# Optimization experiments

Measured on AMD Instinct MI355X. Metric: run time of the kernel, lower is better.

The kernel has to match this reference:

```python
import jax, jax.numpy as jnp
import numpy as np

BLOCK_SIZE = 64
NUM_STEPS = 3
# pad_type='post', init_type='ones', attention_mask=None


def setup_inputs() -> dict:
    key = jax.random.key(0)
    k1, k2, k3 = jax.random.split(key, 3)
    B, H, S, D = 4, 16, 4096, 64
    return {
        "query": jax.random.normal(k1, (B, H, S, D), dtype=jnp.float32),
        "key": jax.random.normal(k2, (B, H, S, D), dtype=jnp.float32),
        "value": jax.random.normal(k3, (B, H, S, D), dtype=jnp.float32),
    }


def _soba_monarch(query, key, value):
    B, H, S, D = query.shape
    bs = BLOCK_SIZE
    nb = -(-S // bs)                 # ceil(S / bs)
    pad = nb * bs - S                # post padding amount
    q = query / (D ** 0.5)

    pad_cfg = ((0, 0), (0, 0), (0, pad), (0, 0))
    Qb = jnp.pad(q, pad_cfg).reshape(B, H, nb, bs, D)      # (l j) v -> l j v
    Kb = jnp.pad(key, pad_cfg).reshape(B, H, nb, bs, D)    # (k i) v -> k i v

    # validity of positions in the padded sequence (post-pad)
    pos_valid = (jnp.arange(nb * bs) < S).reshape(nb, bs)  # [block, within]
    # left factor shape (..., j, l, k): rows of the flattened (l j) axis
    left_mask = jnp.broadcast_to(pos_valid.T[:, :, None], (bs, nb, nb))      # j l k
    # right factor shape (..., k, j, i): columns of the flattened (k i) axis
    right_mask = jnp.broadcast_to(pos_valid[:, None, :], (nb, bs, bs))       # k j i

    NEG = jnp.finfo(q.dtype).min
    # init_type = 'ones'
    left = jnp.broadcast_to(
        jnp.where(left_mask, 1.0 / nb, 0.0), (B, H, bs, nb, nb)
    ).astype(q.dtype)

    for _ in range(NUM_STEPS):
        # beta[k,j,i] = sum_{l,v} left[j,l,k] Q[l,j,v] K[k,i,v]
        beta = jnp.einsum('bhjlk,bhljv,bhkiv->bhkji', left, Qb, Kb, optimize=True)
        tau = jnp.swapaxes(jnp.sum(left, axis=-2), -1, -2)[..., None]        # bhkj1
        tau_zero = jnp.isclose(tau, 0.0)
        tau_safe = jnp.where(tau_zero, 1.0, tau)
        logits_r = jnp.where(right_mask & ~tau_zero, beta / tau_safe, NEG)
        right = jax.nn.softmax(logits_r, axis=-1)
        right = jnp.where(right_mask, right, 0.0)

        # alpha[j,1,k] = sum_i right[k,j,i] log right[k,j,i]  (xlogy)
        r_safe = jnp.where(right > 0, right, 1.0)
        alpha = jnp.sum(right * jnp.log(r_safe), axis=-1)                    # bhkj
        alpha = jnp.swapaxes(alpha, -1, -2)[..., None, :]                    # bhj1k

        beta2 = jnp.einsum('bhkji,bhljv,bhkiv->bhjlk', right, Qb, Kb, optimize=True)
        left = jax.nn.softmax(jnp.where(left_mask, beta2 - alpha, NEG), axis=-1)
        left = jnp.where(left_mask, left, 0.0)

    # multiply: z = L (R V)
    Vb = jnp.pad(value, pad_cfg).reshape(B, H, nb, bs, D)                    # k i v
    Y = jnp.einsum('bhkji,bhkiv->bhkjv', right, Vb)
    Z = jnp.einsum('bhjlk,bhkjv->bhljv', left, Y)
    z = Z.reshape(B, H, nb * bs, D)
    return z[..., :S, :]


def reference(query, key, value):
    return _soba_monarch(query, key, value)
```

## Files before the change

kernel.cpp:

```cpp
#include <hip/hip_runtime.h>


namespace {

typedef __attribute__((ext_vector_type(8))) short short8v;
typedef __attribute__((ext_vector_type(4))) float f32x4;
typedef __attribute__((ext_vector_type(4))) uint uint4v;

constexpr int HEADS = 64;
constexpr size_t HEADQ = 262144;
constexpr size_t MATF  = (size_t)HEADS * 262144;

#define MFMA(ACC, A, B) ACC = __builtin_amdgcn_mfma_f32_16x16x32_bf16(A, B, ACC, 0, 0, 0)

__device__ __forceinline__ float rmax16(float m) {
    m = fmaxf(m, __shfl_xor(m, 1));
    m = fmaxf(m, __shfl_xor(m, 2));
    m = fmaxf(m, __shfl_xor(m, 4));
    m = fmaxf(m, __shfl_xor(m, 8));
    return m;
}
__device__ __forceinline__ float rsum16(float s) {
    s += __shfl_xor(s, 1);
    s += __shfl_xor(s, 2);
    s += __shfl_xor(s, 4);
    s += __shfl_xor(s, 8);
    return s;
}

__device__ __forceinline__ uint packbf(float x) {
    uint u = __float_as_uint(x);
    uint hi = (u + 0x7FFFu + ((u >> 16) & 1u)) & 0xFFFF0000u;
    float d = x - __uint_as_float(hi);
    return hi | (__float_as_uint(d) >> 16);
}

__device__ __forceinline__ void fragpair(const uint* T, int row, int g8,
                                         short8v& h, short8v& l) {
    const uint* p = T + row * 68 + g8 * 8;
    uint4 a = *(const uint4*)(p);
    uint4 b = *(const uint4*)(p + 4);
    uint h01 = (a.x >> 16) | (a.y & 0xFFFF0000u);
    uint h23 = (a.z >> 16) | (a.w & 0xFFFF0000u);
    uint h45 = (b.x >> 16) | (b.y & 0xFFFF0000u);
    uint h67 = (b.z >> 16) | (b.w & 0xFFFF0000u);
    uint l01 = (a.x & 0xFFFFu) | (a.y << 16);
    uint l23 = (a.z & 0xFFFFu) | (a.w << 16);
    uint l45 = (b.x & 0xFFFFu) | (b.y << 16);
    uint l67 = (b.z & 0xFFFFu) | (b.w << 16);
    h = __builtin_bit_cast(short8v, (uint4v){h01, h23, h45, h67});
    l = __builtin_bit_cast(short8v, (uint4v){l01, l23, l45, l67});
}

__global__ void kmean_kernel(const float* __restrict__ Q, uint* __restrict__ M) {
    const int wg = blockIdx.x;
    const int h  = wg >> 6, j = wg & 63;
    const int v  = threadIdx.x;
    const float* base = Q + (size_t)h * HEADQ + (size_t)j * 64 + v;
    float acc = 0.f;
    #pragma unroll
    for (int l = 0; l < 64; ++l) acc += base[(size_t)l * 4096];
    M[(size_t)wg * 64 + v] = packbf(acc * (1.0f / 512.0f));
}

template<int FIRST, int LAST>
__global__ __launch_bounds__(256) void bc_kernel(
    const uint*  __restrict__ Gsrc,
    const float* __restrict__ Kmat,
    const float* __restrict__ Vmat,
    const float* __restrict__ tauIn,
    float* __restrict__ Hm,
    float* __restrict__ alphaOut,
    float* __restrict__ Yout)
{
    __shared__ uint sG[64 * 68];
    __shared__ uint sK[64 * 68];
    __shared__ uint sT[64 * 68];

    const int wg = blockIdx.x, h = wg >> 6, k = wg & 63;
    const int tid = threadIdx.x;
    const int r = tid & 63, c0 = (tid >> 6) << 4;

    {
        const uint* gp = Gsrc + (FIRST ? (size_t)h * 4096 : (size_t)wg * 4096) + r * 64 + c0;
        uint* d = sG + r * 68 + c0;
        #pragma unroll
        for (int q = 0; q < 4; ++q) *(uint4*)(d + 4 * q) = *(const uint4*)(gp + 4 * q);
    }
    {
        const float* kp = Kmat + (size_t)h * HEADQ + (size_t)k * 4096 + r * 64 + c0;
        uint pk[16];
        #pragma unroll
        for (int q = 0; q < 4; ++q) {
            float4 f = *(const float4*)(kp + 4 * q);
            pk[4*q+0] = packbf(f.x); pk[4*q+1] = packbf(f.y);
            pk[4*q+2] = packbf(f.z); pk[4*q+3] = packbf(f.w);
        }
        uint* d = sK + r * 68 + c0;
        #pragma unroll
        for (int q = 0; q < 4; ++q)
            *(uint4*)(d + 4 * q) = *(const uint4*)(&pk[4 * q]);
        #pragma unroll
        for (int e = 0; e < 16; ++e) sT[(c0 + e) * 68 + r] = pk[e];
    }
    float vf[16];
    if (LAST) {
        const float* vp = Vmat + (size_t)h * HEADQ + (size_t)k * 4096 + r * 64 + c0;
        #pragma unroll
        for (int q = 0; q < 4; ++q) {
            float4 f = *(const float4*)(vp + 4 * q);
            vf[4*q+0] = f.x; vf[4*q+1] = f.y; vf[4*q+2] = f.z; vf[4*q+3] = f.w;
        }
    }
    __syncthreads();

    const int w = tid >> 6, lo4 = tid & 15, hi4 = (tid >> 4) & 3;

    f32x4 acc[4] = {};
    #pragma unroll
    for (int ks = 0; ks < 2; ++ks) {
        short8v ah, al; fragpair(sG, 16 * w + lo4, hi4 + 4 * ks, ah, al);
        #pragma unroll
        for (int t = 0; t < 4; ++t) {
            short8v bh, bl; fragpair(sK, 16 * t + lo4, hi4 + 4 * ks, bh, bl);
            MFMA(acc[t], ah, bh); MFMA(acc[t], ah, bl); MFMA(acc[t], al, bh);
        }
    }
    __syncthreads();

    float tvv[4];
    #pragma unroll
    for (int rr = 0; rr < 4; ++rr)
        tvv[rr] = FIRST ? 1.0f : tauIn[(size_t)wg * 64 + 16 * w + 4 * hi4 + rr];

    #pragma unroll
    for (int rr = 0; rr < 4; ++rr) {
        const int j = 16 * w + 4 * hi4 + rr;
        const bool tz = !(tvv[rr] > 1e-8f);
        const float tvi = tz ? 1.0f : (1.0f / tvv[rr]);
        float lg[4];
        #pragma unroll
        for (int t = 0; t < 4; ++t) lg[t] = acc[t][rr] * tvi;
        float m = fmaxf(fmaxf(lg[0], lg[1]), fmaxf(lg[2], lg[3]));
        m = rmax16(m);
        float e[4], s = 0.f;
        #pragma unroll
        for (int t = 0; t < 4; ++t) { e[t] = __expf(lg[t] - m); s += e[t]; }
        s = rsum16(s);
        const float inv = 1.0f / s;
        float ap = 0.f;
        #pragma unroll
        for (int t = 0; t < 4; ++t) {
            const float rrv = tz ? (1.0f / 64.0f) : e[t] * inv;
            ap += (rrv > 0.f) ? rrv * __logf(rrv) : 0.f;
            sG[j * 68 + 16 * t + lo4] = packbf(rrv);
        }
        ap = rsum16(ap);
        if (lo4 == 0) alphaOut[(size_t)wg * 64 + j] = ap;
    }
    if (LAST) {
        #pragma unroll
        for (int e = 0; e < 16; ++e) sK[(c0 + e) * 68 + r] = packbf(vf[e]);
    }
    __syncthreads();

    f32x4 acc2[4] = {};
    f32x4 acc3[4] = {};
    #pragma unroll
    for (int ks = 0; ks < 2; ++ks) {
        short8v ah, al; fragpair(sG, 16 * w + lo4, hi4 + 4 * ks, ah, al);
        #pragma unroll
        for (int t = 0; t < 4; ++t) {
            short8v bh, bl; fragpair(sT, 16 * t + lo4, hi4 + 4 * ks, bh, bl);
            MFMA(acc2[t], ah, bh); MFMA(acc2[t], ah, bl); MFMA(acc2[t], al, bh);
            if (LAST) {
                short8v ch, cl; fragpair(sK, 16 * t + lo4, hi4 + 4 * ks, ch, cl);
                MFMA(acc3[t], ah, ch); MFMA(acc3[t], ah, cl); MFMA(acc3[t], al, ch);
            }
        }
    }
    #pragma unroll
    for (int rr = 0; rr < 4; ++rr) {
        const int j = 16 * w + 4 * hi4 + rr;
        const size_t base = (size_t)h * 262144 + (size_t)j * 4096 + (size_t)k * 64;
        #pragma unroll
        for (int t = 0; t < 4; ++t) {
            Hm[base + 16 * t + lo4] = acc2[t][rr];
            if (LAST) Yout[base + 16 * t + lo4] = acc3[t][rr];
        }
    }
}

template<int LAST>
__global__ __launch_bounds__(256) void da_kernel(
    const float* __restrict__ Q,
    const float* __restrict__ HmIn,
    const float* __restrict__ alphaIn,
    const float* __restrict__ Yin,
    uint*  __restrict__ Gout,
    float* __restrict__ tauOut,
    float* __restrict__ Zout)
{
    __shared__ uint sQ[64 * 68];
    __shared__ uint sH[64 * 68];
    __shared__ uint sT[64 * 68];

    const int wg = blockIdx.x, h = wg >> 6, j = wg & 63;
    const int tid = threadIdx.x;
    const int r = tid & 63, c0 = (tid >> 6) << 4;

    {
        const float* qp = Q + (size_t)h * HEADQ + (size_t)r * 4096 + (size_t)j * 64 + c0;
        uint pq[16];
        #pragma unroll
        for (int q = 0; q < 4; ++q) {
            float4 f = *(const float4*)(qp + 4 * q);
            pq[4*q+0] = packbf(f.x * 0.125f); pq[4*q+1] = packbf(f.y * 0.125f);
            pq[4*q+2] = packbf(f.z * 0.125f); pq[4*q+3] = packbf(f.w * 0.125f);
        }
        uint* d = sQ + r * 68 + c0;
        #pragma unroll
        for (int q = 0; q < 4; ++q)
            *(uint4*)(d + 4 * q) = *(const uint4*)(&pq[4 * q]);
        if (!LAST) {
            #pragma unroll
            for (int e = 0; e < 16; ++e) sT[(c0 + e) * 68 + r] = pq[e];
        }
    }
    {
        const float* hp = HmIn + (size_t)wg * 4096 + r * 64 + c0;
        uint ph[16];
        #pragma unroll
        for (int q = 0; q < 4; ++q) {
            float4 f = *(const float4*)(hp + 4 * q);
            ph[4*q+0] = packbf(f.x); ph[4*q+1] = packbf(f.y);
            ph[4*q+2] = packbf(f.z); ph[4*q+3] = packbf(f.w);
        }
        uint* d = sH + r * 68 + c0;
        #pragma unroll
        for (int q = 0; q < 4; ++q)
            *(uint4*)(d + 4 * q) = *(const uint4*)(&ph[4 * q]);
    }
    if (LAST) {
        const float* yp = Yin + (size_t)wg * 4096 + r * 64 + c0;
        float yf[16];
        #pragma unroll
        for (int q = 0; q < 4; ++q) {
            float4 f = *(const float4*)(yp + 4 * q);
            yf[4*q+0] = f.x; yf[4*q+1] = f.y; yf[4*q+2] = f.z; yf[4*q+3] = f.w;
        }
        #pragma unroll
        for (int e = 0; e < 16; ++e) sT[(c0 + e) * 68 + r] = packbf(yf[e]);
    }
    __syncthreads();

    const int w = tid >> 6, lo4 = tid & 15, hi4 = (tid >> 4) & 3;

    f32x4 acc[4] = {};
    #pragma unroll
    for (int ks = 0; ks < 2; ++ks) {
        short8v ah, al; fragpair(sQ, 16 * w + lo4, hi4 + 4 * ks, ah, al);
        #pragma unroll
        for (int t = 0; t < 4; ++t) {
            short8v bh, bl; fragpair(sH, 16 * t + lo4, hi4 + 4 * ks, bh, bl);
            MFMA(acc[t], ah, bh); MFMA(acc[t], ah, bl); MFMA(acc[t], al, bh);
        }
    }
    __syncthreads();

    float av[4];
    #pragma unroll
    for (int t = 0; t < 4; ++t)
        av[t] = alphaIn[((size_t)h * 64 + 16 * t + lo4) * 64 + j];

    #pragma unroll
    for (int rr = 0; rr < 4; ++rr) {
        const int l = 16 * w + 4 * hi4 + rr;
        float lg[4];
        #pragma unroll
        for (int t = 0; t < 4; ++t) lg[t] = acc[t][rr] - av[t];
        float m = fmaxf(fmaxf(lg[0], lg[1]), fmaxf(lg[2], lg[3]));
        m = rmax16(m);
        float e[4], s = 0.f;
        #pragma unroll
        for (int t = 0; t < 4; ++t) { e[t] = __expf(lg[t] - m); s += e[t]; }
        s = rsum16(s);
        const float inv = 1.0f / s;
        #pragma unroll
        for (int t = 0; t < 4; ++t) {
            const uint pv = packbf(e[t] * inv);
            if (!LAST) sH[(16 * t + lo4) * 68 + l] = pv;
            else       sH[l * 68 + 16 * t + lo4] = pv;
        }
    }
    __syncthreads();

    if (!LAST) {
        f32x4 acc2[4] = {};
        f32x4 tacc = {};
        short8v onesb;
        #pragma unroll
        for (int e = 0; e < 8; ++e) onesb[e] = (lo4 == 0) ? (short)0x3F80 : (short)0;
        #pragma unroll
        for (int ks = 0; ks < 2; ++ks) {
            short8v ah, al; fragpair(sH, 16 * w + lo4, hi4 + 4 * ks, ah, al);
            MFMA(tacc, ah, onesb); MFMA(tacc, al, onesb);
            #pragma unroll
            for (int t = 0; t < 4; ++t) {
                short8v bh, bl; fragpair(sT, 16 * t + lo4, hi4 + 4 * ks, bh, bl);
                MFMA(acc2[t], ah, bh); MFMA(acc2[t], ah, bl); MFMA(acc2[t], al, bh);
            }
        }
        #pragma unroll
        for (int rr = 0; rr < 4; ++rr) {
            const int kq = 16 * w + 4 * hi4 + rr;
            const size_t gb = ((size_t)h * 64 + kq) * 4096 + (size_t)j * 64;
            #pragma unroll
            for (int t = 0; t < 4; ++t) Gout[gb + 16 * t + lo4] = packbf(acc2[t][rr]);
            if (lo4 == 0) tauOut[((size_t)h * 64 + kq) * 64 + j] = tacc[rr];
        }
    } else {
        f32x4 acc2[4] = {};
        #pragma unroll
        for (int ks = 0; ks < 2; ++ks) {
            short8v ah, al; fragpair(sH, 16 * w + lo4, hi4 + 4 * ks, ah, al);
            #pragma unroll
            for (int t = 0; t < 4; ++t) {
                short8v bh, bl; fragpair(sT, 16 * t + lo4, hi4 + 4 * ks, bh, bl);
                MFMA(acc2[t], ah, bh); MFMA(acc2[t], ah, bl); MFMA(acc2[t], al, bh);
            }
        }
        #pragma unroll
        for (int rr = 0; rr < 4; ++rr) {
            const int l = 16 * w + 4 * hi4 + rr;
            const size_t zb = (size_t)h * HEADQ + (size_t)l * 4096 + (size_t)j * 64;
            #pragma unroll
            for (int t = 0; t < 4; ++t) Zout[zb + 16 * t + lo4] = acc2[t][rr];
        }
    }
}

}

extern "C" void kernel_launch(void* const* d_in, const int* in_sizes, int n_in,
                              void* d_out, int out_size, void* d_ws, size_t ws_size,
                              hipStream_t stream) {
    const float* Q = (const float*)d_in[0];
    const float* K = (const float*)d_in[1];
    const float* V = (const float*)d_in[2];
    float* out = (float*)d_out;

    char* ws = (char*)d_ws;
    const size_t MB = 1024 * 1024;
    uint*  G   = (uint*)(ws);
    float* Hm  = (float*)(ws + 64 * MB);
    uint*  M   = (uint*)(ws + 128 * MB);
    float* al  = (float*)(ws + 129 * MB);
    float* tau = (float*)(ws + 130 * MB);

    const bool bigws = ws_size >= (size_t)196 * MB;
    float* Ybuf = bigws ? (float*)(ws + 131 * MB) : out;
    float* Zdst = bigws ? out : (float*)G;

    dim3 blk(256), grid(HEADS * 64);

    kmean_kernel<<<dim3(HEADS * 64), dim3(64), 0, stream>>>(Q, M);
    bc_kernel<1, 0><<<grid, blk, 0, stream>>>(M, K, nullptr, nullptr, Hm, al, nullptr);
    da_kernel<0>   <<<grid, blk, 0, stream>>>(Q, Hm, al, nullptr, G, tau, nullptr);
    bc_kernel<0, 0><<<grid, blk, 0, stream>>>(G, K, nullptr, tau, Hm, al, nullptr);
    da_kernel<0>   <<<grid, blk, 0, stream>>>(Q, Hm, al, nullptr, G, tau, nullptr);
    bc_kernel<0, 1><<<grid, blk, 0, stream>>>(G, K, V, tau, Hm, al, Ybuf);
    da_kernel<1>   <<<grid, blk, 0, stream>>>(Q, Hm, al, Ybuf, nullptr, nullptr, Zdst);
    if (!bigws)
        hipMemcpyAsync(d_out, G, MATF * sizeof(float), hipMemcpyDeviceToDevice, stream);
}
```

Measured before the change: 331.3 us.

## Store split-bf16 hi/lo planes in LDS and coalesce intermediate global writes

Shared-memory tiles now hold separate hi and lo bf16 planes with a stride of 72, so MFMA fragments come from direct 16-byte loads and no longer need per-fragment unpacking. Intermediates Hm and Y are stored as packed hi/lo uint instead of fp32, and all outputs (Hm, Y, G, Z) are staged through LDS before being written to global memory. Together with transposed addressing, this makes global stores and loads coalesced. In exchange the kernel uses more barriers and reuses LDS buffers, and the LAST path gets an extra matmul phase with its own syncs.

After: 305.5 us. 7.8% less time.

```diff
diff --git a/kernel.cpp b/kernel.cpp
--- a/kernel.cpp
+++ b/kernel.cpp
@@ -5,13 +5,13 @@
 
 typedef __attribute__((ext_vector_type(8))) short short8v;
 typedef __attribute__((ext_vector_type(4))) float f32x4;
-typedef __attribute__((ext_vector_type(4))) uint uint4v;
 
 constexpr int HEADS = 64;
 constexpr size_t HEADQ = 262144;
 constexpr size_t MATF  = (size_t)HEADS * 262144;
 
 #define MFMA(ACC, A, B) ACC = __builtin_amdgcn_mfma_f32_16x16x32_bf16(A, B, ACC, 0, 0, 0)
+#define LD8(arr, row, g8) (*(const short8v*)((arr) + (row) * 72 + (g8) * 8))
 
 __device__ __forceinline__ float rmax16(float m) {
     m = fmaxf(m, __shfl_xor(m, 1));
@@ -28,28 +28,96 @@
     return s;
 }
 
+__device__ __forceinline__ void bfsplit(float x, ushort& h, ushort& l) {
+    uint u = __float_as_uint(x);
+    uint hi = (u + 0x7FFFu + ((u >> 16) & 1u)) & 0xFFFF0000u;
+    h = (ushort)(hi >> 16);
+    l = (ushort)(__float_as_uint(x - __uint_as_float(hi)) >> 16);
+}
 __device__ __forceinline__ uint packbf(float x) {
     uint u = __float_as_uint(x);
     uint hi = (u + 0x7FFFu + ((u >> 16) & 1u)) & 0xFFFF0000u;
-    float d = x - __uint_as_float(hi);
-    return hi | (__float_as_uint(d) >> 16);
-}
-
-__device__ __forceinline__ void fragpair(const uint* T, int row, int g8,
-                                         short8v& h, short8v& l) {
-    const uint* p = T + row * 68 + g8 * 8;
-    uint4 a = *(const uint4*)(p);
-    uint4 b = *(const uint4*)(p + 4);
-    uint h01 = (a.x >> 16) | (a.y & 0xFFFF0000u);
-    uint h23 = (a.z >> 16) | (a.w & 0xFFFF0000u);
-    uint h45 = (b.x >> 16) | (b.y & 0xFFFF0000u);
-    uint h67 = (b.z >> 16) | (b.w & 0xFFFF0000u);
-    uint l01 = (a.x & 0xFFFFu) | (a.y << 16);
-    uint l23 = (a.z & 0xFFFFu) | (a.w << 16);
-    uint l45 = (b.x & 0xFFFFu) | (b.y << 16);
-    uint l67 = (b.z & 0xFFFFu) | (b.w << 16);
-    h = __builtin_bit_cast(short8v, (uint4v){h01, h23, h45, h67});
-    l = __builtin_bit_cast(short8v, (uint4v){l01, l23, l45, l67});
+    return hi | (__float_as_uint(x - __uint_as_float(hi)) >> 16);
+}
+
+struct Frag16 { short8v h0, h1, l0, l1; };
+
+__device__ __forceinline__ Frag16 load_packed16(const uint* p) {
+    Frag16 f;
+    #pragma unroll
+    for (int q = 0; q < 4; ++q) {
+        uint4 a = *(const uint4*)(p + 4 * q);
+        uint vv[4] = {a.x, a.y, a.z, a.w};
+        #pragma unroll
+        for (int e = 0; e < 4; ++e) {
+            const int i = 4 * q + e;
+            const ushort hh = (ushort)(vv[e] >> 16), ll = (ushort)(vv[e] & 0xFFFFu);
+            if (i < 8) { f.h0[i] = (short)hh; f.l0[i] = (short)ll; }
+            else       { f.h1[i - 8] = (short)hh; f.l1[i - 8] = (short)ll; }
+        }
+    }
+    return f;
+}
+__device__ __forceinline__ Frag16 load_f32x16(const float* p, float s) {
+    Frag16 f;
+    #pragma unroll
+    for (int q = 0; q < 4; ++q) {
+        float4 a = *(const float4*)(p + 4 * q);
+        float vv[4] = {a.x * s, a.y * s, a.z * s, a.w * s};
+        #pragma unroll
+        for (int e = 0; e < 4; ++e) {
+            const int i = 4 * q + e;
+            ushort hh, ll; bfsplit(vv[e], hh, ll);
+            if (i < 8) { f.h0[i] = (short)hh; f.l0[i] = (short)ll; }
+            else       { f.h1[i - 8] = (short)hh; f.l1[i - 8] = (short)ll; }
+        }
+    }
+    return f;
+}
+__device__ __forceinline__ void store_rows(ushort* H, ushort* L, int r, int c0,
+                                           const Frag16& f) {
+    *(short8v*)(H + r * 72 + c0)     = f.h0;
+    *(short8v*)(H + r * 72 + c0 + 8) = f.h1;
+    *(short8v*)(L + r * 72 + c0)     = f.l0;
+    *(short8v*)(L + r * 72 + c0 + 8) = f.l1;
+}
+__device__ __forceinline__ void scatter_tr(ushort* H, ushort* L, int r, int c0,
+                                           const Frag16& f) {
+    #pragma unroll
+    for (int e = 0; e < 8; ++e) {
+        H[(c0 + e) * 72 + r] = (ushort)f.h0[e];
+        L[(c0 + e) * 72 + r] = (ushort)f.l0[e];
+    }
+    #pragma unroll
+    for (int e = 0; e < 8; ++e) {
+        H[(c0 + 8 + e) * 72 + r] = (ushort)f.h1[e];
+        L[(c0 + 8 + e) * 72 + r] = (ushort)f.l1[e];
+    }
+}
+
+__device__ __forceinline__ void flush_u32(const uint* OS, uint* g, int tid) {
+    #pragma unroll
+    for (int q = 0; q < 4; ++q) {
+        const int off = tid * 4 + q * 1024;
+        uint4 v = *(const uint4*)(OS + (off >> 6) * 68 + (off & 63));
+        *(uint4*)(g + off) = v;
+    }
+}
+
+__device__ __forceinline__ void mmstep(const ushort* AH, const ushort* AL,
+                                       const ushort* BH, const ushort* BL,
+                                       int w, int lo4, int hi4, f32x4 acc[4]) {
+    #pragma unroll
+    for (int ks = 0; ks < 2; ++ks) {
+        short8v ah = LD8(AH, 16 * w + lo4, hi4 + 4 * ks);
+        short8v al = LD8(AL, 16 * w + lo4, hi4 + 4 * ks);
+        #pragma unroll
+        for (int t = 0; t < 4; ++t) {
+            short8v bh = LD8(BH, 16 * t + lo4, hi4 + 4 * ks);
+            short8v bl = LD8(BL, 16 * t + lo4, hi4 + 4 * ks);
+            MFMA(acc[t], ah, bh); MFMA(acc[t], ah, bl); MFMA(acc[t], al, bh);
+        }
+    }
 }
 
 __global__ void kmean_kernel(const float* __restrict__ Q, uint* __restrict__ M) {
@@ -69,209 +137,141 @@
     const float* __restrict__ Kmat,
     const float* __restrict__ Vmat,
     const float* __restrict__ tauIn,
-    float* __restrict__ Hm,
+    uint*  __restrict__ HmOut,
     float* __restrict__ alphaOut,
-    float* __restrict__ Yout)
+    uint*  __restrict__ Yout)
 {
-    __shared__ uint sG[64 * 68];
-    __shared__ uint sK[64 * 68];
-    __shared__ uint sT[64 * 68];
+    __shared__ uint SM[9216];
+    ushort* Ah = (ushort*)SM;        ushort* Al = Ah + 4608;
+    ushort* Bh = (ushort*)(SM + 4608); ushort* Bl = Bh + 4608;
+    uint* OS  = SM + 4608;
+    uint* OS2 = SM;
 
     const int wg = blockIdx.x, h = wg >> 6, k = wg & 63;
-    const int tid = threadIdx.x;
-    const int r = tid & 63, c0 = (tid >> 6) << 4;
+    const int tid = threadIdx.x, r = tid & 63, c0 = (tid >> 6) << 4;
 
     {
-        const uint* gp = Gsrc + (FIRST ? (size_t)h * 4096 : (size_t)wg * 4096) + r * 64 + c0;
-        uint* d = sG + r * 68 + c0;
-        #pragma unroll
-        for (int q = 0; q < 4; ++q) *(uint4*)(d + 4 * q) = *(const uint4*)(gp + 4 * q);
-    }
-    {
-        const float* kp = Kmat + (size_t)h * HEADQ + (size_t)k * 4096 + r * 64 + c0;
-        uint pk[16];
-        #pragma unroll
-        for (int q = 0; q < 4; ++q) {
-            float4 f = *(const float4*)(kp + 4 * q);
-            pk[4*q+0] = packbf(f.x); pk[4*q+1] = packbf(f.y);
-            pk[4*q+2] = packbf(f.z); pk[4*q+3] = packbf(f.w);
-        }
-        uint* d = sK + r * 68 + c0;
-        #pragma unroll
-        for (int q = 0; q < 4; ++q)
-            *(uint4*)(d + 4 * q) = *(const uint4*)(&pk[4 * q]);
-        #pragma unroll
-        for (int e = 0; e < 16; ++e) sT[(c0 + e) * 68 + r] = pk[e];
-    }
-    float vf[16];
-    if (LAST) {
-        const float* vp = Vmat + (size_t)h * HEADQ + (size_t)k * 4096 + r * 64 + c0;
-        #pragma unroll
-        for (int q = 0; q < 4; ++q) {
-            float4 f = *(const float4*)(vp + 4 * q);
-            vf[4*q+0] = f.x; vf[4*q+1] = f.y; vf[4*q+2] = f.z; vf[4*q+3] = f.w;
-        }
-    }
-    __syncthreads();
+        const uint* gp = FIRST ? (Gsrc + ((size_t)h * 64 + r) * 64 + c0)
+                               : (Gsrc + ((size_t)h * 64 + r) * 4096 + (size_t)k * 64 + c0);
+        Frag16 fg = load_packed16(gp);
+        store_rows(Ah, Al, r, c0, fg);
+    }
+    Frag16 fk = load_f32x16(Kmat + (size_t)h * HEADQ + (size_t)k * 4096 + r * 64 + c0, 1.f);
+    store_rows(Bh, Bl, r, c0, fk);
+    Frag16 fv;
+    if (LAST)
+        fv = load_f32x16(Vmat + (size_t)h * HEADQ + (size_t)k * 4096 + r * 64 + c0, 1.f);
 
     const int w = tid >> 6, lo4 = tid & 15, hi4 = (tid >> 4) & 3;
+    float tvv[4];
+    #pragma unroll
+    for (int rr = 0; rr < 4; ++rr)
+        tvv[rr] = FIRST ? 1.f : tauIn[((size_t)h * 64 + k) * 64 + 16 * w + 4 * hi4 + rr];
+    __syncthreads();
 
     f32x4 acc[4] = {};
-    #pragma unroll
-    for (int ks = 0; ks < 2; ++ks) {
-        short8v ah, al; fragpair(sG, 16 * w + lo4, hi4 + 4 * ks, ah, al);
-        #pragma unroll
-        for (int t = 0; t < 4; ++t) {
-            short8v bh, bl; fragpair(sK, 16 * t + lo4, hi4 + 4 * ks, bh, bl);
-            MFMA(acc[t], ah, bh); MFMA(acc[t], ah, bl); MFMA(acc[t], al, bh);
-        }
-    }
-    __syncthreads();
-
-    float tvv[4];
-    #pragma unroll
-    for (int rr = 0; rr < 4; ++rr)
-        tvv[rr] = FIRST ? 1.0f : tauIn[(size_t)wg * 64 + 16 * w + 4 * hi4 + rr];
+    mmstep(Ah, Al, Bh, Bl, w, lo4, hi4, acc);
+    __syncthreads();
 
     #pragma unroll
     for (int rr = 0; rr < 4; ++rr) {
         const int j = 16 * w + 4 * hi4 + rr;
         const bool tz = !(tvv[rr] > 1e-8f);
-        const float tvi = tz ? 1.0f : (1.0f / tvv[rr]);
+        const float tvi = tz ? 1.f : 1.f / tvv[rr];
         float lg[4];
         #pragma unroll
         for (int t = 0; t < 4; ++t) lg[t] = acc[t][rr] * tvi;
-        float m = fmaxf(fmaxf(lg[0], lg[1]), fmaxf(lg[2], lg[3]));
-        m = rmax16(m);
+        float m = rmax16(fmaxf(fmaxf(lg[0], lg[1]), fmaxf(lg[2], lg[3])));
         float e[4], s = 0.f;
         #pragma unroll
         for (int t = 0; t < 4; ++t) { e[t] = __expf(lg[t] - m); s += e[t]; }
         s = rsum16(s);
-        const float inv = 1.0f / s;
+        const float inv = 1.f / s;
         float ap = 0.f;
         #pragma unroll
         for (int t = 0; t < 4; ++t) {
-            const float rrv = tz ? (1.0f / 64.0f) : e[t] * inv;
-            ap += (rrv > 0.f) ? rrv * __logf(rrv) : 0.f;
-            sG[j * 68 + 16 * t + lo4] = packbf(rrv);
+            const float rv = tz ? (1.f / 64.f) : e[t] * inv;
+            ap += (rv > 0.f) ? rv * __logf(rv) : 0.f;
+            ushort hh, ll; bfsplit(rv, hh, ll);
+            Ah[j * 72 + 16 * t + lo4] = hh;
+            Al[j * 72 + 16 * t + lo4] = ll;
         }
         ap = rsum16(ap);
-        if (lo4 == 0) alphaOut[(size_t)wg * 64 + j] = ap;
-    }
+        if (lo4 == 0) alphaOut[((size_t)h * 64 + j) * 64 + k] = ap;
+    }
+    scatter_tr(Bh, Bl, r, c0, fk);
+    __syncthreads();
+
+    f32x4 acc2[4] = {};
+    mmstep(Ah, Al, Bh, Bl, w, lo4, hi4, acc2);
+    f32x4 acc3[4] = {};
     if (LAST) {
-        #pragma unroll
-        for (int e = 0; e < 16; ++e) sK[(c0 + e) * 68 + r] = packbf(vf[e]);
-    }
-    __syncthreads();
-
-    f32x4 acc2[4] = {};
-    f32x4 acc3[4] = {};
-    #pragma unroll
-    for (int ks = 0; ks < 2; ++ks) {
-        short8v ah, al; fragpair(sG, 16 * w + lo4, hi4 + 4 * ks, ah, al);
-        #pragma unroll
-        for (int t = 0; t < 4; ++t) {
-            short8v bh, bl; fragpair(sT, 16 * t + lo4, hi4 + 4 * ks, bh, bl);
-            MFMA(acc2[t], ah, bh); MFMA(acc2[t], ah, bl); MFMA(acc2[t], al, bh);
-            if (LAST) {
-                short8v ch, cl; fragpair(sK, 16 * t + lo4, hi4 + 4 * ks, ch, cl);
-                MFMA(acc3[t], ah, ch); MFMA(acc3[t], ah, cl); MFMA(acc3[t], al, ch);
-            }
-        }
-    }
+        __syncthreads();
+        scatter_tr(Bh, Bl, r, c0, fv);
+        __syncthreads();
+        mmstep(Ah, Al, Bh, Bl, w, lo4, hi4, acc3);
+    }
+    __syncthreads();
+
     #pragma unroll
     for (int rr = 0; rr < 4; ++rr) {
         const int j = 16 * w + 4 * hi4 + rr;
-        const size_t base = (size_t)h * 262144 + (size_t)j * 4096 + (size_t)k * 64;
-        #pragma unroll
-        for (int t = 0; t < 4; ++t) {
-            Hm[base + 16 * t + lo4] = acc2[t][rr];
-            if (LAST) Yout[base + 16 * t + lo4] = acc3[t][rr];
-        }
-    }
+        #pragma unroll
+        for (int t = 0; t < 4; ++t) OS[j * 68 + 16 * t + lo4] = packbf(acc2[t][rr]);
+    }
+    if (LAST) {
+        #pragma unroll
+        for (int rr = 0; rr < 4; ++rr) {
+            const int j = 16 * w + 4 * hi4 + rr;
+            #pragma unroll
+            for (int t = 0; t < 4; ++t) OS2[j * 68 + 16 * t + lo4] = packbf(acc3[t][rr]);
+        }
+    }
+    __syncthreads();
+    flush_u32(OS, HmOut + (size_t)wg * 4096, tid);
+    if (LAST) flush_u32(OS2, Yout + (size_t)wg * 4096, tid);
 }
 
 template<int LAST>
 __global__ __launch_bounds__(256) void da_kernel(
     const float* __restrict__ Q,
-    const float* __restrict__ HmIn,
+    const uint*  __restrict__ HmIn,
     const float* __restrict__ alphaIn,
-    const float* __restrict__ Yin,
+    const uint*  __restrict__ Yin,
     uint*  __restrict__ Gout,
     float* __restrict__ tauOut,
     float* __restrict__ Zout)
 {
-    __shared__ uint sQ[64 * 68];
-    __shared__ uint sH[64 * 68];
-    __shared__ uint sT[64 * 68];
+    __shared__ uint SM[9216];
+    ushort* Ah = (ushort*)SM;        ushort* Al = Ah + 4608;
+    ushort* Bh = (ushort*)(SM + 4608); ushort* Bl = Bh + 4608;
+    uint*  OSu = SM + 4608;
+    float* OSf = (float*)(SM + 4608);
 
     const int wg = blockIdx.x, h = wg >> 6, j = wg & 63;
-    const int tid = threadIdx.x;
-    const int r = tid & 63, c0 = (tid >> 6) << 4;
-
+    const int tid = threadIdx.x, r = tid & 63, c0 = (tid >> 6) << 4;
+
+    Frag16 fq = load_f32x16(Q + (size_t)h * HEADQ + (size_t)r * 4096 + (size_t)j * 64 + c0,
+                            0.125f);
+    store_rows(Ah, Al, r, c0, fq);
     {
-        const float* qp = Q + (size_t)h * HEADQ + (size_t)r * 4096 + (size_t)j * 64 + c0;
-        uint pq[16];
-        #pragma unroll
-        for (int q = 0; q < 4; ++q) {
-            float4 f = *(const float4*)(qp + 4 * q);
-            pq[4*q+0] = packbf(f.x * 0.125f); pq[4*q+1] = packbf(f.y * 0.125f);
-            pq[4*q+2] = packbf(f.z * 0.125f); pq[4*q+3] = packbf(f.w * 0.125f);
-        }
-        uint* d = sQ + r * 68 + c0;
-        #pragma unroll
-        for (int q = 0; q < 4; ++q)
-            *(uint4*)(d + 4 * q) = *(const uint4*)(&pq[4 * q]);
-        if (!LAST) {
-            #pragma unroll
-            for (int e = 0; e < 16; ++e) sT[(c0 + e) * 68 + r] = pq[e];
-        }
-    }
-    {
-        const float* hp = HmIn + (size_t)wg * 4096 + r * 64 + c0;
-        uint ph[16];
-        #pragma unroll
-        for (int q = 0; q < 4; ++q) {
-            float4 f = *(const float4*)(hp + 4 * q);
-            ph[4*q+0] = packbf(f.x); ph[4*q+1] = packbf(f.y);
-            ph[4*q+2] = packbf(f.z); ph[4*q+3] = packbf(f.w);
-        }
-        uint* d = sH + r * 68 + c0;
-        #pragma unroll
-        for (int q = 0; q < 4; ++q)
-            *(uint4*)(d + 4 * q) = *(const uint4*)(&ph[4 * q]);
-    }
-    if (LAST) {
-        const float* yp = Yin + (size_t)wg * 4096 + r * 64 + c0;
-        float yf[16];
-        #pragma unroll
-        for (int q = 0; q < 4; ++q) {
-            float4 f = *(const float4*)(yp + 4 * q);
-            yf[4*q+0] = f.x; yf[4*q+1] = f.y; yf[4*q+2] = f.z; yf[4*q+3] = f.w;
-        }
-        #pragma unroll
-        for (int e = 0; e < 16; ++e) sT[(c0 + e) * 68 + r] = packbf(yf[e]);
-    }
-    __syncthreads();
+        Frag16 fh = load_packed16(HmIn + ((size_t)h * 64 + r) * 4096 + (size_t)j * 64 + c0);
+        store_rows(Bh, Bl, r, c0, fh);
+    }
+    Frag16 fy;
+    if (LAST)
+        fy = load_packed16(Yin + ((size_t)h * 64 + r) * 4096 + (size_t)j * 64 + c0);
 
     const int w = tid >> 6, lo4 = tid & 15, hi4 = (tid >> 4) & 3;
+    float av[4];
+    #pragma unroll
+    for (int t = 0; t < 4; ++t)
+        av[t] = alphaIn[((size_t)h * 64 + j) * 64 + 16 * t + lo4];
+    __syncthreads();
 
     f32x4 acc[4] = {};
-    #pragma unroll
-    for (int ks = 0; ks < 2; ++ks) {
-        short8v ah, al; fragpair(sQ, 16 * w + lo4, hi4 + 4 * ks, ah, al);
-        #pragma unroll
-        for (int t = 0; t < 4; ++t) {
-            short8v bh, bl; fragpair(sH, 16 * t + lo4, hi4 + 4 * ks, bh, bl);
-            MFMA(acc[t], ah, bh); MFMA(acc[t], ah, bl); MFMA(acc[t], al, bh);
-        }
-    }
-    __syncthreads();
-
-    float av[4];
-    #pragma unroll
-    for (int t = 0; t < 4; ++t)
-        av[t] = alphaIn[((size_t)h * 64 + 16 * t + lo4) * 64 + j];
+    mmstep(Ah, Al, Bh, Bl, w, lo4, hi4, acc);
+    __syncthreads();
 
     #pragma unroll
     for (int rr = 0; rr < 4; ++rr) {
@@ -279,20 +279,22 @@
         float lg[4];
         #pragma unroll
         for (int t = 0; t < 4; ++t) lg[t] = acc[t][rr] - av[t];
-        float m = fmaxf(fmaxf(lg[0], lg[1]), fmaxf(lg[2], lg[3]));
-        m = rmax16(m);
+        float m = rmax16(fmaxf(fmaxf(lg[0], lg[1]), fmaxf(lg[2], lg[3])));
         float e[4], s = 0.f;
         #pragma unroll
         for (int t = 0; t < 4; ++t) { e[t] = __expf(lg[t] - m); s += e[t]; }
         s = rsum16(s);
-        const float inv = 1.0f / s;
+        const float inv = 1.f / s;
         #pragma unroll
         for (int t = 0; t < 4; ++t) {
-            const uint pv = packbf(e[t] * inv);
-            if (!LAST) sH[(16 * t + lo4) * 68 + l] = pv;
-            else       sH[l * 68 + 16 * t + lo4] = pv;
-        }
-    }
+            const float lv = e[t] * inv;
+            ushort hh, ll; bfsplit(lv, hh, ll);
+            if (!LAST) { Bh[(16 * t + lo4) * 72 + l] = hh; Bl[(16 * t + lo4) * 72 + l] = ll; }
+            else       { Bh[l * 72 + 16 * t + lo4] = hh; Bl[l * 72 + 16 * t + lo4] = ll; }
+        }
+    }
+    if (!LAST) scatter_tr(Ah, Al, r, c0, fq);
+    else       scatter_tr(Ah, Al, r, c0, fy);
     __syncthreads();
 
     if (!LAST) {
@@ -300,42 +302,56 @@
         f32x4 tacc = {};
         short8v onesb;
         #pragma unroll
-        for (int e = 0; e < 8; ++e) onesb[e] = (lo4 == 0) ? (short)0x3F80 : (short)0;
+        for (int e2 = 0; e2 < 8; ++e2) onesb[e2] = (lo4 == 0) ? (short)0x3F80 : (short)0;
         #pragma unroll
         for (int ks = 0; ks < 2; ++ks) {
-            short8v ah, al; fragpair(sH, 16 * w + lo4, hi4 + 4 * ks, ah, al);
+            short8v ah = LD8(Bh, 16 * w + lo4, hi4 + 4 * ks);
+            short8v al = LD8(Bl, 16 * w + lo4, hi4 + 4 * ks);
             MFMA(tacc, ah, onesb); MFMA(tacc, al, onesb);
             #pragma unroll
             for (int t = 0; t < 4; ++t) {
-                short8v bh, bl; fragpair(sT, 16 * t + lo4, hi4 + 4 * ks, bh, bl);
+                short8v bh = LD8(Ah, 16 * t + lo4, hi4 + 4 * ks);
+                short8v bl = LD8(Al, 16 * t + lo4, hi4 + 4 * ks);
                 MFMA(acc2[t], ah, bh); MFMA(acc2[t], ah, bl); MFMA(acc2[t], al, bh);
             }
         }
+        __syncthreads();
         #pragma unroll
         for (int rr = 0; rr < 4; ++rr) {
             const int kq = 16 * w + 4 * hi4 + rr;
-            const size_t gb = ((size_t)h * 64 + kq) * 4096 + (size_t)j * 64;
-            #pragma unroll
-            for (int t = 0; t < 4; ++t) Gout[gb + 16 * t + lo4] = packbf(acc2[t][rr]);
             if (lo4 == 0) tauOut[((size_t)h * 64 + kq) * 64 + j] = tacc[rr];
-        }
+            #pragma unroll
+            for (int t = 0; t < 4; ++t) OSu[kq * 68 + 16 * t + lo4] = packbf(acc2[t][rr]);
+        }
+        __syncthreads();
+        flush_u32(OSu, Gout + (size_t)wg * 4096, tid);
     } else {
         f32x4 acc2[4] = {};
         #pragma unroll
         for (int ks = 0; ks < 2; ++ks) {
-            short8v ah, al; fragpair(sH, 16 * w + lo4, hi4 + 4 * ks, ah, al);
+            short8v ah = LD8(Bh, 16 * w + lo4, hi4 + 4 * ks);
+            short8v al = LD8(Bl, 16 * w + lo4, hi4 + 4 * ks);
             #pragma unroll
             for (int t = 0; t < 4; ++t) {
-                short8v bh, bl; fragpair(sT, 16 * t + lo4, hi4 + 4 * ks, bh, bl);
+                short8v bh = LD8(Ah, 16 * t + lo4, hi4 + 4 * ks);
+                short8v bl = LD8(Al, 16 * t + lo4, hi4 + 4 * ks);
                 MFMA(acc2[t], ah, bh); MFMA(acc2[t], ah, bl); MFMA(acc2[t], al, bh);
             }
         }
+        __syncthreads();
         #pragma unroll
         for (int rr = 0; rr < 4; ++rr) {
             const int l = 16 * w + 4 * hi4 + rr;
-            const size_t zb = (size_t)h * HEADQ + (size_t)l * 4096 + (size_t)j * 64;
-            #pragma unroll
-            for (int t = 0; t < 4; ++t) Zout[zb + 16 * t + lo4] = acc2[t][rr];
+            #pragma unroll
+            for (int t = 0; t < 4; ++t) OSf[l * 68 + 16 * t + lo4] = acc2[t][rr];
+        }
+        __syncthreads();
+        #pragma unroll
+        for (int q = 0; q < 4; ++q) {
+            const int l = (tid >> 4) + 16 * q;
+            const int v4 = (tid & 15) * 4;
+            float4 vv = *(const float4*)(OSf + l * 68 + v4);
+            *(float4*)(Zout + (size_t)h * HEADQ + (size_t)l * 4096 + (size_t)j * 64 + v4) = vv;
         }
     }
 }
@@ -353,13 +369,13 @@
     char* ws = (char*)d_ws;
     const size_t MB = 1024 * 1024;
     uint*  G   = (uint*)(ws);
-    float* Hm  = (float*)(ws + 64 * MB);
+    uint*  Hm  = (uint*)(ws + 64 * MB);
     uint*  M   = (uint*)(ws + 128 * MB);
     float* al  = (float*)(ws + 129 * MB);
     float* tau = (float*)(ws + 130 * MB);
 
     const bool bigws = ws_size >= (size_t)196 * MB;
-    float* Ybuf = bigws ? (float*)(ws + 131 * MB) : out;
+    uint*  Ybuf = bigws ? (uint*)(ws + 131 * MB) : (uint*)out;
     float* Zdst = bigws ? out : (float*)G;
 
     dim3 blk(256), grid(HEADS * 64);
```
